# Optimization experiments

Measured on AMD Instinct MI355X. Metric: run time of the kernel, lower is better.

Reference implementation:

```python
import jax, jax.numpy as jnp
import numpy as np

VOCAB, EMB, HID, NCLS = 50257, 48, 128, 2000
B, S = 512, 1024


def setup_inputs() -> dict:
    key = jax.random.key(0)
    ks = jax.random.split(key, 8)
    x = jax.random.randint(ks[0], (B, S), 0, VOCAB)
    emb_table = jax.random.normal(ks[1], (VOCAB, EMB), dtype=jnp.float32)
    emb_table = emb_table.at[0].set(0.0)  # padding_idx=0
    k_ih = 1.0 / np.sqrt(HID)
    w_ih = jax.random.uniform(ks[2], (4 * HID, EMB), minval=-k_ih, maxval=k_ih, dtype=jnp.float32)
    w_hh = jax.random.uniform(ks[3], (4 * HID, HID), minval=-k_ih, maxval=k_ih, dtype=jnp.float32)
    b_ih = jax.random.uniform(ks[4], (4 * HID,), minval=-k_ih, maxval=k_ih, dtype=jnp.float32)
    b_hh = jax.random.uniform(ks[5], (4 * HID,), minval=-k_ih, maxval=k_ih, dtype=jnp.float32)
    k_fc = 1.0 / np.sqrt(HID)
    w_fc = jax.random.uniform(ks[6], (NCLS, HID), minval=-k_fc, maxval=k_fc, dtype=jnp.float32)
    b_fc = jax.random.uniform(ks[7], (NCLS,), minval=-k_fc, maxval=k_fc, dtype=jnp.float32)
    return {"x": x, "emb_table": emb_table, "w_ih": w_ih, "w_hh": w_hh,
            "b_ih": b_ih, "b_hh": b_hh, "w_fc": w_fc, "b_fc": b_fc}


def _lstm_last_hidden(e, w_ih, w_hh, b_ih, b_hh):
    # e: [B, S, E]. Precompute input contributions for all timesteps (one big GEMM).
    xg = jnp.einsum('bse,ge->bsg', e, w_ih) + b_ih + b_hh  # [B, S, 4H]
    xg = jnp.transpose(xg, (1, 0, 2))                      # [S, B, 4H]
    Bn = e.shape[0]
    h0 = jnp.zeros((Bn, HID), e.dtype)
    c0 = jnp.zeros((Bn, HID), e.dtype)

    def step(carry, xg_t):
        h, c = carry
        g = xg_t + h @ w_hh.T                              # [B, 4H]
        i, f, gg, o = jnp.split(g, 4, axis=-1)             # PyTorch gate order i,f,g,o
        i = jax.nn.sigmoid(i)
        f = jax.nn.sigmoid(f)
        gg = jnp.tanh(gg)
        o = jax.nn.sigmoid(o)
        c = f * c + i * gg
        h = o * jnp.tanh(c)
        return (h, c), None

    (h_n, _), _ = jax.lax.scan(step, (h0, c0), xg)
    return h_n


def reference(x, emb_table, w_ih, w_hh, b_ih, b_hh, w_fc, b_fc):
    e = emb_table[x]                                       # [B, S, E] gather
    h_n = _lstm_last_hidden(e, w_ih, w_hh, b_ih, b_hh)     # [B, H]
    return h_n @ w_fc.T + b_fc                             # [B, NCLS]
```

## Files before the change

### kernel.cpp

```cpp
#include <hip/hip_runtime.h>

#define DI __device__ __forceinline__

typedef unsigned int uint;
typedef unsigned short ushort;
typedef _Float16 half2t __attribute__((ext_vector_type(2)));
typedef _Float16 f16x8 __attribute__((ext_vector_type(8)));
typedef float f32x4 __attribute__((ext_vector_type(4)));

#define VOCAB 50257
#define NEMB 48
#define HID 128
#define G4 512
#define NCLS 2000
#define BATCH 512
#define SEQ 1024
#define MROWS 2
#define NBLK2 (BATCH / MROWS)

DI float sigm(float x) {
  return __builtin_amdgcn_rcpf(1.0f + __builtin_amdgcn_exp2f(-1.4426950408889634f * x));
}
DI float tanhfast(float x) {
  return 1.0f - 2.0f * __builtin_amdgcn_rcpf(__builtin_amdgcn_exp2f(2.8853900817779268f * x) + 1.0f);
}

DI void barrier_lds_only() {
  asm volatile("s_waitcnt lgkmcnt(0)" ::: "memory");
  __builtin_amdgcn_s_barrier();
  asm volatile("" ::: "memory");
}

#define VROWS 32
__global__ __launch_bounds__(512) void build_P(
    const float* __restrict__ emb, const float* __restrict__ w_ih,
    const float* __restrict__ b_ih, const float* __restrict__ b_hh,
    _Float16* __restrict__ P)
{
  __shared__ __align__(16) float eL[VROWS][NEMB];
  const int tid = threadIdx.x;
  const int v0 = blockIdx.x * VROWS;
  int nrows = VOCAB - v0; if (nrows > VROWS) nrows = VROWS;

  for (int f = tid; f < nrows * NEMB; f += 512)
    eL[f / NEMB][f % NEMB] = emb[(size_t)v0 * NEMB + f];

  float w[NEMB];
  {
    const float* wr = w_ih + (size_t)tid * NEMB;
#pragma unroll
    for (int k = 0; k < NEMB; k++) w[k] = wr[k];
  }
  float bias = b_ih[tid] + b_hh[tid];
  const int pidx = ((tid & 127) << 2) + (tid >> 7);
  __syncthreads();

  for (int v = 0; v < nrows; v++) {
    const float4* e4 = (const float4*)&eL[v][0];
    float a = bias;
#pragma unroll
    for (int k = 0; k < NEMB / 4; k++) {
      float4 e = e4[k];
      a += w[4 * k] * e.x + w[4 * k + 1] * e.y + w[4 * k + 2] * e.z + w[4 * k + 3] * e.w;
    }
    P[(size_t)(v0 + v) * G4 + pidx] = (_Float16)a;
  }
}

__global__ __launch_bounds__(512, 2) void lstm_mfma2(
    const int* __restrict__ x, const float* __restrict__ w_hh,
    const _Float16* __restrict__ P, float* __restrict__ hout)
{
  __shared__ ushort tokL[MROWS][SEQ];
  __shared__ __align__(16) _Float16 hbuf[16][HID];
  __shared__ __align__(8) float2 gpair[G4];

  const int tid  = threadIdx.x;
  const int lane = tid & 63;
  const int wave = tid >> 6;
  const int l15  = lane & 15;
  const int lg   = lane >> 4;
  const int blk  = blockIdx.x;

  {
    const int* xp = x + (size_t)blk * MROWS * SEQ;
    for (int i = tid; i < MROWS * SEQ; i += 512) ((ushort*)tokL)[i] = (ushort)xp[i];
  }
  for (int i = tid; i < 16 * HID / 2; i += 512) ((uint*)hbuf)[i] = 0u;

  f16x8 Bf[4][4];
#pragma unroll
  for (int tau = 0; tau < 4; tau++) {
    const float* wr = w_hh + (size_t)(wave * 64 + tau * 16 + l15) * HID + lg * 8;
#pragma unroll
    for (int ck = 0; ck < 4; ck++) {
      const float4* p4 = (const float4*)(wr + ck * 32);
      float4 wa = p4[0], wb = p4[1];
      f16x8 f;
      f[0] = (_Float16)wa.x; f[1] = (_Float16)wa.y;
      f[2] = (_Float16)wa.z; f[3] = (_Float16)wa.w;
      f[4] = (_Float16)wb.x; f[5] = (_Float16)wb.y;
      f[6] = (_Float16)wb.z; f[7] = (_Float16)wb.w;
      Bf[tau][ck] = f;
    }
  }

  int aoff[4];
#pragma unroll
  for (int ck = 0; ck < 4; ck++)
    aoff[ck] = l15 * 256 + ((((ck * 4 + lg) ^ l15)) << 4);

  const int grow = tid >> 7;
  const int gcol = tid & 127;
  const int gbase = gcol * 2 + grow;
  const int hwoff = grow * 256 + (((gcol >> 3) ^ grow) << 4) + (gcol & 7) * 2;
  float cst = 0.0f;

  __syncthreads();

  uint2 xgA = {0, 0}, xgB = {0, 0};
  if (tid < 256) {
    int t0 = tokL[grow][0], t1 = tokL[grow][1];
    xgA = *(const uint2*)(P + (size_t)t0 * G4 + gcol * 4);
    xgB = *(const uint2*)(P + (size_t)t1 * G4 + gcol * 4);
  }

  const f32x4 fz = {0.f, 0.f, 0.f, 0.f};
  const char* hB = (const char*)hbuf;

#define MF(Areg, ckk, a0, a1, a2, a3) do {                                     \
    a0 = __builtin_amdgcn_mfma_f32_16x16x32_f16(Areg, Bf[0][ckk], a0, 0, 0, 0);\
    a1 = __builtin_amdgcn_mfma_f32_16x16x32_f16(Areg, Bf[1][ckk], a1, 0, 0, 0);\
    a2 = __builtin_amdgcn_mfma_f32_16x16x32_f16(Areg, Bf[2][ckk], a2, 0, 0, 0);\
    a3 = __builtin_amdgcn_mfma_f32_16x16x32_f16(Areg, Bf[3][ckk], a3, 0, 0, 0);\
  } while (0)

#define STEP(t, par) do {                                                      \
    f16x8 A0 = *(const f16x8*)(hB + aoff[0]);                                  \
    f16x8 A1 = *(const f16x8*)(hB + aoff[1]);                                  \
    f16x8 A2 = *(const f16x8*)(hB + aoff[2]);                                  \
    f16x8 A3 = *(const f16x8*)(hB + aoff[3]);                                  \
    f32x4 a0 = fz, a1 = fz, a2 = fz, a3 = fz;                                  \
    MF(A0, 0, a0, a1, a2, a3);                                                 \
    MF(A1, 1, a0, a1, a2, a3);                                                 \
    MF(A2, 2, a0, a1, a2, a3);                                                 \
    MF(A3, 3, a0, a1, a2, a3);                                                 \
    uint2 xcur = {0, 0};                                                       \
    if (tid < 256) {                                                           \
      xcur = (par) ? xgB : xgA;       \
      int tc = (t) + 2; if (tc > SEQ - 1) tc = SEQ - 1;                        \
      int tk = tokL[grow][tc];                                                 \
      uint2 v = *(const uint2*)(P + (size_t)tk * G4 + gcol * 4);               \
      if (par) xgB = v; else xgA = v;                                          \
    }                                                                          \
    if (lg == 0) { \
      float2 p;                                                                \
      p.x = a0[0]; p.y = a0[1]; gpair[wave * 64 +  0 + l15] = p;               \
      p.x = a1[0]; p.y = a1[1]; gpair[wave * 64 + 16 + l15] = p;               \
      p.x = a2[0]; p.y = a2[1]; gpair[wave * 64 + 32 + l15] = p;               \
      p.x = a3[0]; p.y = a3[1]; gpair[wave * 64 + 48 + l15] = p;               \
    }                                                                          \
    barrier_lds_only();                                                        \
    if (tid < 256) {                                                           \
      half2t x0 = __builtin_bit_cast(half2t, xcur.x);                          \
      half2t x1 = __builtin_bit_cast(half2t, xcur.y);                          \
      const float* gp = (const float*)gpair;                                   \
      float gi = gp[gbase]       + (float)x0.x;                                \
      float gf = gp[gbase + 256] + (float)x0.y;                                \
      float gc = gp[gbase + 512] + (float)x1.x;                                \
      float go = gp[gbase + 768] + (float)x1.y;                                \
      float fi = sigm(gi), ff = sigm(gf), gt = tanhfast(gc), fo = sigm(go);    \
      cst = ff * cst + fi * gt;                                                \
      float hh = fo * tanhfast(cst);                                           \
      *(_Float16*)((char*)hbuf + hwoff) = (_Float16)hh;                        \
      if ((t) == SEQ - 1)                                                      \
        hout[((size_t)blk * MROWS + grow) * HID + gcol] = hh;                  \
    }                                                                          \
    barrier_lds_only();                                                        \
  } while (0)

  for (int t = 0; t < SEQ; t += 2) { STEP(t, 0); STEP(t + 1, 1); }
#undef STEP
#undef MF
}

typedef _Float16 h2 __attribute__((ext_vector_type(2)));
DI float fdot2f(h2 a, h2 b, float c) { return c + (float)a.x * (float)b.x + (float)a.y * (float)b.y; }

__global__ __launch_bounds__(512, 4) void lstm_scan_fb(
    const int* __restrict__ x, const float* __restrict__ emb,
    const float* __restrict__ w_ih, const float* __restrict__ w_hh,
    const float* __restrict__ b_ih, const float* __restrict__ b_hh,
    float* __restrict__ hout)
{
  __shared__ int tokL[SEQ];
  __shared__ __align__(16) _Float16 h16[HID];
  __shared__ float g2h[2][G4];
  __shared__ __align__(8) h2 e16[2][NEMB / 2];

  const int tid = threadIdx.x;
  const int b = blockIdx.x;
  const int col = tid & 255;
  const int kh = tid >> 8;
  const int koff = kh * (HID / 2);

  {
    const int* xp = x + (size_t)b * SEQ;
#pragma unroll
    for (int i = 0; i < SEQ / 512; i++) tokL[tid + 512 * i] = xp[tid + 512 * i];
  }

  h2 w0[HID / 4], w1[HID / 4];
  {
    const float4* wr0 = (const float4*)(w_hh + (size_t)col * HID + koff);
    const float4* wr1 = (const float4*)(w_hh + (size_t)(col + 256) * HID + koff);
#pragma unroll
    for (int k = 0; k < HID / 8; k++) {
      float4 a = wr0[k];
      h2 p; p.x = (_Float16)a.x; p.y = (_Float16)a.y; w0[2 * k] = p;
      p.x = (_Float16)a.z; p.y = (_Float16)a.w; w0[2 * k + 1] = p;
      float4 bv = wr1[k];
      p.x = (_Float16)bv.x; p.y = (_Float16)bv.y; w1[2 * k] = p;
      p.x = (_Float16)bv.z; p.y = (_Float16)bv.w; w1[2 * k + 1] = p;
    }
  }
  h2 wih0[NEMB / 2], wih1[NEMB / 2];
  float bias0 = 0.0f, bias1 = 0.0f;
  if (kh == 0) {
    const float* wr0 = w_ih + (size_t)col * NEMB;
    const float* wr1 = w_ih + (size_t)(col + 256) * NEMB;
#pragma unroll
    for (int k = 0; k < NEMB / 2; k++) {
      h2 p;
      p.x = (_Float16)wr0[2 * k]; p.y = (_Float16)wr0[2 * k + 1]; wih0[k] = p;
      p.x = (_Float16)wr1[2 * k]; p.y = (_Float16)wr1[2 * k + 1]; wih1[k] = p;
    }
    bias0 = b_ih[col] + b_hh[col];
    bias1 = b_ih[col + 256] + b_hh[col + 256];
  }
  if (tid < HID) h16[tid] = (_Float16)0.0f;
  __syncthreads();

  float c = 0.0f;
  float2 einfl = {0.0f, 0.0f};
  if (tid < NEMB / 2) {
    float2 e0 = ((const float2*)(emb + (size_t)tokL[0] * NEMB))[tid];
    einfl    = ((const float2*)(emb + (size_t)tokL[1] * NEMB))[tid];
    h2 p; p.x = (_Float16)e0.x; p.y = (_Float16)e0.y;
    e16[0][tid] = p;
  }
  __syncthreads();

#define STEPF(t, par) do {                                                     \
    float xg0, xg1;                                                            \
    if (tid < NEMB / 2) {                                                      \
      int tc = (t) + 2; if (tc > SEQ - 1) tc = SEQ - 1;                        \
      h2 p; p.x = (_Float16)einfl.x; p.y = (_Float16)einfl.y;                  \
      e16[((t) + 1) & 1][tid] = p;                                             \
      einfl = ((const float2*)(emb + (size_t)tokL[tc] * NEMB))[tid];           \
    }                                                                          \
    if (kh == 0) {                                                             \
      xg0 = bias0; xg1 = bias1;                                                \
      _Pragma("unroll")                                                        \
      for (int k = 0; k < NEMB / 2; k++) {                                     \
        xg0 = fdot2f(wih0[k], e16[(par)][k], xg0);                             \
        xg1 = fdot2f(wih1[k], e16[(par)][k], xg1);                             \
      }                                                                        \
    } else { xg0 = 0.0f; xg1 = 0.0f; }                                         \
    const uint4* hv = (const uint4*)h16 + (kh << 3);                           \
    float s0 = xg0, u0 = 0.0f, s1 = xg1, u1 = 0.0f;                            \
    _Pragma("unroll")                                                          \
    for (int kt = 0; kt < HID / 16; kt++) {                                    \
      uint4 hq = hv[kt];                                                       \
      h2 ha = __builtin_bit_cast(h2, hq.x);                                    \
      h2 hb = __builtin_bit_cast(h2, hq.y);                                    \
      h2 hc = __builtin_bit_cast(h2, hq.z);                                    \
      h2 hd = __builtin_bit_cast(h2, hq.w);                                    \
      s0 = fdot2f(w0[4 * kt + 0], ha, s0);                                     \
      u0 = fdot2f(w0[4 * kt + 1], hb, u0);                                     \
      s0 = fdot2f(w0[4 * kt + 2], hc, s0);                                     \
      u0 = fdot2f(w0[4 * kt + 3], hd, u0);                                     \
      s1 = fdot2f(w1[4 * kt + 0], ha, s1);                                     \
      u1 = fdot2f(w1[4 * kt + 1], hb, u1);                                     \
      s1 = fdot2f(w1[4 * kt + 2], hc, s1);                                     \
      u1 = fdot2f(w1[4 * kt + 3], hd, u1);                                     \
    }                                                                          \
    g2h[kh][col] = s0 + u0;                                                    \
    g2h[kh][col + 256] = s1 + u1;                                              \
    barrier_lds_only();                                                        \
    if (tid < HID) {                                                           \
      float gi = g2h[0][tid]           + g2h[1][tid];                          \
      float gf = g2h[0][HID + tid]     + g2h[1][HID + tid];                    \
      float gc = g2h[0][2 * HID + tid] + g2h[1][2 * HID + tid];                \
      float go = g2h[0][3 * HID + tid] + g2h[1][3 * HID + tid];                \
      float fi = sigm(gi), ff = sigm(gf), gt = tanhfast(gc), fo = sigm(go);    \
      c = ff * c + fi * gt;                                                    \
      float hh = fo * tanhfast(c);                                             \
      h16[tid] = (_Float16)hh;                                                 \
      if ((t) == SEQ - 1) hout[(size_t)b * HID + tid] = hh;                    \
    }                                                                          \
    barrier_lds_only();                                                        \
  } while (0)

  for (int t = 0; t < SEQ; t += 2) { STEPF(t, 0); STEPF(t + 1, 1); }
#undef STEPF
}

#define FCR 64
#define FCC 64
__global__ __launch_bounds__(256) void fc_kernel(
    const float* __restrict__ h, const float* __restrict__ w_fc,
    const float* __restrict__ b_fc, float* __restrict__ out)
{
  __shared__ float aT[HID][FCR];
  __shared__ float bT[HID][FCC];
  const int tid = threadIdx.x;
  const int r0 = blockIdx.y * FCR;
  const int c0 = blockIdx.x * FCC;

  for (int f = tid; f < FCR * (HID / 4); f += 256) {
    int row = f >> 5, q = f & 31;
    float4 v = ((const float4*)h)[(((size_t)(r0 + row)) << 5) + q];
    aT[4 * q + 0][row] = v.x; aT[4 * q + 1][row] = v.y;
    aT[4 * q + 2][row] = v.z; aT[4 * q + 3][row] = v.w;
    int wrow = c0 + row;
    float4 wv;
    if (wrow < NCLS) wv = ((const float4*)w_fc)[(((size_t)wrow) << 5) + q];
    else { wv.x = 0.f; wv.y = 0.f; wv.z = 0.f; wv.w = 0.f; }
    bT[4 * q + 0][row] = wv.x; bT[4 * q + 1][row] = wv.y;
    bT[4 * q + 2][row] = wv.z; bT[4 * q + 3][row] = wv.w;
  }
  __syncthreads();

  const int cr = tid & 15, rr = tid >> 4;
  float acc[4][4];
#pragma unroll
  for (int i = 0; i < 4; i++)
#pragma unroll
    for (int j = 0; j < 4; j++) acc[i][j] = 0.0f;

#pragma unroll 4
  for (int k = 0; k < HID; k++) {
    float4 av = *(const float4*)&aT[k][4 * rr];
    float4 bv = *(const float4*)&bT[k][4 * cr];
    float a[4] = {av.x, av.y, av.z, av.w};
    float bb[4] = {bv.x, bv.y, bv.z, bv.w};
#pragma unroll
    for (int i = 0; i < 4; i++)
#pragma unroll
      for (int j = 0; j < 4; j++) acc[i][j] += a[i] * bb[j];
  }

#pragma unroll
  for (int j = 0; j < 4; j++) {
    int cc = c0 + 4 * cr + j;
    if (cc < NCLS) {
      float bias = b_fc[cc];
#pragma unroll
      for (int i = 0; i < 4; i++)
        out[(size_t)(r0 + 4 * rr + i) * NCLS + cc] = acc[i][j] + bias;
    }
  }
}

extern "C" void kernel_launch(void* const* d_in, const int* in_sizes, int n_in,
                              void* d_out, int out_size, void* d_ws, size_t ws_size,
                              hipStream_t stream) {
  const int*   xx   = (const int*)d_in[0];
  const float* emb  = (const float*)d_in[1];
  const float* w_ih = (const float*)d_in[2];
  const float* w_hh = (const float*)d_in[3];
  const float* b_ih = (const float*)d_in[4];
  const float* b_hh = (const float*)d_in[5];
  const float* w_fc = (const float*)d_in[6];
  const float* b_fc = (const float*)d_in[7];
  float* out = (float*)d_out;

  const size_t pbytes = (size_t)VOCAB * G4 * sizeof(_Float16);
  const size_t palign = (pbytes + 255) & ~(size_t)255;
  const size_t hbytes = (size_t)BATCH * HID * sizeof(float);

  float* hout;
  if (ws_size >= palign + hbytes) {
    _Float16* P = (_Float16*)d_ws;
    hout = (float*)((char*)d_ws + palign);
    build_P<<<(VOCAB + VROWS - 1) / VROWS, 512, 0, stream>>>(emb, w_ih, b_ih, b_hh, P);
    lstm_mfma2<<<NBLK2, 512, 0, stream>>>(xx, w_hh, P, hout);
  } else {
    hout = (float*)d_ws;
    lstm_scan_fb<<<BATCH, 512, 0, stream>>>(xx, emb, w_ih, w_hh, b_ih, b_hh, hout);
  }
  dim3 fcg((NCLS + FCC - 1) / FCC, BATCH / FCR);
  fc_kernel<<<fcg, 256, 0, stream>>>(hout, w_fc, b_fc, out);
}
```

Before: 916.1 us.

## Remap LSTM gate columns per wave and double-buffer hidden state to drop a barrier

The w_hh column assignment is remapped so each wave's four MFMA accumulators hold the i, f, g and o gates of the same hidden unit. The lane that computes a unit can then apply the cell update directly from its registers, with no exchange of gate pre-activations through LDS. The hidden state is double-buffered in LDS, which removes one of the two block barriers per timestep and the gpair round trip. In exchange, the elementwise work now runs on only 16 lanes per wave, each handling two batch rows serially, so those lanes carry a longer serial section each step.

Result: faster. 869.0 us (-5.1%).

```diff
diff --git a/kernel.cpp b/kernel.cpp
--- a/kernel.cpp
+++ b/kernel.cpp
@@ -67,31 +67,34 @@
   }
 }
 
-__global__ __launch_bounds__(512, 2) void lstm_mfma2(
+__global__ __launch_bounds__(512, 2) void lstm_mfma4(
     const int* __restrict__ x, const float* __restrict__ w_hh,
     const _Float16* __restrict__ P, float* __restrict__ hout)
 {
   __shared__ ushort tokL[MROWS][SEQ];
-  __shared__ __align__(16) _Float16 hbuf[16][HID];
-  __shared__ __align__(8) float2 gpair[G4];
+  __shared__ __align__(16) _Float16 hbuf[2][16][HID];
 
   const int tid  = threadIdx.x;
   const int lane = tid & 63;
   const int wave = tid >> 6;
   const int l15  = lane & 15;
   const int lg   = lane >> 4;
+  const int u    = wave * 16 + l15;
   const int blk  = blockIdx.x;
 
   {
     const int* xp = x + (size_t)blk * MROWS * SEQ;
     for (int i = tid; i < MROWS * SEQ; i += 512) ((ushort*)tokL)[i] = (ushort)xp[i];
   }
-  for (int i = tid; i < 16 * HID / 2; i += 512) ((uint*)hbuf)[i] = 0u;
+  {
+    uint4 z; z.x = z.y = z.z = z.w = 0u;
+    ((uint4*)hbuf)[tid] = z;
+  }
 
   f16x8 Bf[4][4];
 #pragma unroll
-  for (int tau = 0; tau < 4; tau++) {
-    const float* wr = w_hh + (size_t)(wave * 64 + tau * 16 + l15) * HID + lg * 8;
+  for (int g = 0; g < 4; g++) {
+    const float* wr = w_hh + (size_t)(g * 128 + u) * HID + lg * 8;
 #pragma unroll
     for (int ck = 0; ck < 4; ck++) {
       const float4* p4 = (const float4*)(wr + ck * 32);
@@ -101,7 +104,7 @@
       f[2] = (_Float16)wa.z; f[3] = (_Float16)wa.w;
       f[4] = (_Float16)wb.x; f[5] = (_Float16)wb.y;
       f[6] = (_Float16)wb.z; f[7] = (_Float16)wb.w;
-      Bf[tau][ck] = f;
+      Bf[g][ck] = f;
     }
   }
 
@@ -110,23 +113,23 @@
   for (int ck = 0; ck < 4; ck++)
     aoff[ck] = l15 * 256 + ((((ck * 4 + lg) ^ l15)) << 4);
 
-  const int grow = tid >> 7;
-  const int gcol = tid & 127;
-  const int gbase = gcol * 2 + grow;
-  const int hwoff = grow * 256 + (((gcol >> 3) ^ grow) << 4) + (gcol & 7) * 2;
-  float cst = 0.0f;
+  const int hwoff0 = u * 2;
+  const int hwoff1 = 256 + ((((u >> 3) ^ 1)) << 4) + (u & 7) * 2;
+  float cst0 = 0.0f, cst1 = 0.0f;
 
   __syncthreads();
 
-  uint2 xgA = {0, 0}, xgB = {0, 0};
-  if (tid < 256) {
-    int t0 = tokL[grow][0], t1 = tokL[grow][1];
-    xgA = *(const uint2*)(P + (size_t)t0 * G4 + gcol * 4);
-    xgB = *(const uint2*)(P + (size_t)t1 * G4 + gcol * 4);
+  uint2 xgA0 = {0,0}, xgA1 = {0,0}, xgB0 = {0,0}, xgB1 = {0,0};
+  if (lg == 0) {
+    xgA0 = *(const uint2*)(P + (size_t)tokL[0][0] * G4 + u * 4);
+    xgA1 = *(const uint2*)(P + (size_t)tokL[1][0] * G4 + u * 4);
+    xgB0 = *(const uint2*)(P + (size_t)tokL[0][1] * G4 + u * 4);
+    xgB1 = *(const uint2*)(P + (size_t)tokL[1][1] * G4 + u * 4);
   }
 
   const f32x4 fz = {0.f, 0.f, 0.f, 0.f};
   const char* hB = (const char*)hbuf;
+  char* hW = (char*)hbuf;
 
 #define MF(Areg, ckk, a0, a1, a2, a3) do {                                     \
     a0 = __builtin_amdgcn_mfma_f32_16x16x32_f16(Areg, Bf[0][ckk], a0, 0, 0, 0);\
@@ -136,45 +139,55 @@
   } while (0)
 
 #define STEP(t, par) do {                                                      \
-    f16x8 A0 = *(const f16x8*)(hB + aoff[0]);                                  \
-    f16x8 A1 = *(const f16x8*)(hB + aoff[1]);                                  \
-    f16x8 A2 = *(const f16x8*)(hB + aoff[2]);                                  \
-    f16x8 A3 = *(const f16x8*)(hB + aoff[3]);                                  \
+    const char* hc = hB + (par) * 4096;                                        \
+    f16x8 A0 = *(const f16x8*)(hc + aoff[0]);                                  \
+    f16x8 A1 = *(const f16x8*)(hc + aoff[1]);                                  \
+    f16x8 A2 = *(const f16x8*)(hc + aoff[2]);                                  \
+    f16x8 A3 = *(const f16x8*)(hc + aoff[3]);                                  \
     f32x4 a0 = fz, a1 = fz, a2 = fz, a3 = fz;                                  \
     MF(A0, 0, a0, a1, a2, a3);                                                 \
     MF(A1, 1, a0, a1, a2, a3);                                                 \
     MF(A2, 2, a0, a1, a2, a3);                                                 \
     MF(A3, 3, a0, a1, a2, a3);                                                 \
-    uint2 xcur = {0, 0};                                                       \
-    if (tid < 256) {                                                           \
-      xcur = (par) ? xgB : xgA;       \
+    if (lg == 0) {                                                             \
+      uint2 xc0 = (par) ? xgB0 : xgA0;           \
+      uint2 xc1 = (par) ? xgB1 : xgA1;                                         \
       int tc = (t) + 2; if (tc > SEQ - 1) tc = SEQ - 1;                        \
-      int tk = tokL[grow][tc];                                                 \
-      uint2 v = *(const uint2*)(P + (size_t)tk * G4 + gcol * 4);               \
-      if (par) xgB = v; else xgA = v;                                          \
-    }                                                                          \
-    if (lg == 0) { \
-      float2 p;                                                                \
-      p.x = a0[0]; p.y = a0[1]; gpair[wave * 64 +  0 + l15] = p;               \
-      p.x = a1[0]; p.y = a1[1]; gpair[wave * 64 + 16 + l15] = p;               \
-      p.x = a2[0]; p.y = a2[1]; gpair[wave * 64 + 32 + l15] = p;               \
-      p.x = a3[0]; p.y = a3[1]; gpair[wave * 64 + 48 + l15] = p;               \
-    }                                                                          \
-    barrier_lds_only();                                                        \
-    if (tid < 256) {                                                           \
-      half2t x0 = __builtin_bit_cast(half2t, xcur.x);                          \
-      half2t x1 = __builtin_bit_cast(half2t, xcur.y);                          \
-      const float* gp = (const float*)gpair;                                   \
-      float gi = gp[gbase]       + (float)x0.x;                                \
-      float gf = gp[gbase + 256] + (float)x0.y;                                \
-      float gc = gp[gbase + 512] + (float)x1.x;                                \
-      float go = gp[gbase + 768] + (float)x1.y;                                \
-      float fi = sigm(gi), ff = sigm(gf), gt = tanhfast(gc), fo = sigm(go);    \
-      cst = ff * cst + fi * gt;                                                \
-      float hh = fo * tanhfast(cst);                                           \
-      *(_Float16*)((char*)hbuf + hwoff) = (_Float16)hh;                        \
-      if ((t) == SEQ - 1)                                                      \
-        hout[((size_t)blk * MROWS + grow) * HID + gcol] = hh;                  \
+      int tk0 = tokL[0][tc], tk1 = tokL[1][tc];                                \
+      uint2 v0 = *(const uint2*)(P + (size_t)tk0 * G4 + u * 4);                \
+      uint2 v1 = *(const uint2*)(P + (size_t)tk1 * G4 + u * 4);                \
+      if (par) { xgB0 = v0; xgB1 = v1; } else { xgA0 = v0; xgA1 = v1; }        \
+      char* hn = hW + ((par) ^ 1) * 4096;                                      \
+                                                    \
+      {                                                                        \
+        half2t x0 = __builtin_bit_cast(half2t, xc0.x);                         \
+        half2t x1 = __builtin_bit_cast(half2t, xc0.y);                         \
+        float gi = a0[0] + (float)x0.x;                                        \
+        float gf = a1[0] + (float)x0.y;                                        \
+        float gc = a2[0] + (float)x1.x;                                        \
+        float go = a3[0] + (float)x1.y;                                        \
+        float fi = sigm(gi), ff = sigm(gf), gt = tanhfast(gc), fo = sigm(go);  \
+        cst0 = ff * cst0 + fi * gt;                                            \
+        float hh = fo * tanhfast(cst0);                                        \
+        *(_Float16*)(hn + hwoff0) = (_Float16)hh;                              \
+        if ((t) == SEQ - 1)                                                    \
+          hout[((size_t)blk * MROWS + 0) * HID + u] = hh;                      \
+      }                                                                        \
+                                                    \
+      {                                                                        \
+        half2t x0 = __builtin_bit_cast(half2t, xc1.x);                         \
+        half2t x1 = __builtin_bit_cast(half2t, xc1.y);                         \
+        float gi = a0[1] + (float)x0.x;                                        \
+        float gf = a1[1] + (float)x0.y;                                        \
+        float gc = a2[1] + (float)x1.x;                                        \
+        float go = a3[1] + (float)x1.y;                                        \
+        float fi = sigm(gi), ff = sigm(gf), gt = tanhfast(gc), fo = sigm(go);  \
+        cst1 = ff * cst1 + fi * gt;                                            \
+        float hh = fo * tanhfast(cst1);                                        \
+        *(_Float16*)(hn + hwoff1) = (_Float16)hh;                              \
+        if ((t) == SEQ - 1)                                                    \
+          hout[((size_t)blk * MROWS + 1) * HID + u] = hh;                      \
+      }                                                                        \
     }                                                                          \
     barrier_lds_only();                                                        \
   } while (0)
@@ -385,7 +398,7 @@
     _Float16* P = (_Float16*)d_ws;
     hout = (float*)((char*)d_ws + palign);
     build_P<<<(VOCAB + VROWS - 1) / VROWS, 512, 0, stream>>>(emb, w_ih, b_ih, b_hh, P);
-    lstm_mfma2<<<NBLK2, 512, 0, stream>>>(xx, w_hh, P, hout);
+    lstm_mfma4<<<NBLK2, 512, 0, stream>>>(xx, w_hh, P, hout);
   } else {
     hout = (float*)d_ws;
     lstm_scan_fb<<<BATCH, 512, 0, stream>>>(xx, emb, w_ih, w_hh, b_ih, b_hh, hout);
```
